# Optimization experiments

Hardware: AMD Instinct MI355X
Metric: run time of the kernel (lower is better)

Reference implementation:

```python
import jax, jax.numpy as jnp
import numpy as np

N_WIN = 7  # winsize in PSF.forward
EMBED_DIM = 3
N_EMBED = 8192

def _box_sum(x, n=N_WIN):
    # sliding-window sum with zero padding == torch ZeroPad2d + unfold sum
    C = x.shape[1]
    k = jnp.ones((C, 1, n, n), x.dtype)
    return jax.lax.conv_general_dilated(
        x, k, (1, 1), [(n // 2, n // 2)] * 2,
        feature_group_count=C, dimension_numbers=('NCHW', 'OIHW', 'NCHW'))

def _patch_stats(x, n=N_WIN):
    # mean / unbiased var over the n*n window (zeros included, matching unfold of zero-padded input)
    N = n * n
    s1 = _box_sum(x, n)
    s2 = _box_sum(x * x, n)
    mean = s1 / N
    var = (s2 - s1 * s1 / N) / (N - 1)  # torch .var default unbiased=True
    return mean, var

def _patch_mv_norm(x, n=N_WIN):
    m, v = _patch_stats(x, n)
    return (x - m) / (jnp.sqrt(v) + 1e-8)

def _conv1x1(x, w, b):
    return jnp.einsum('oi,bihw->bohw', w, x) + b[None, :, None, None]

def _ln(x, g, b, eps=1e-5):
    m = x.mean(-1, keepdims=True)
    v = x.var(-1, keepdims=True)
    return (x - m) / jnp.sqrt(v + eps) * g + b

def _mlp(x, w1, b1, w2, b2):
    h = jax.nn.gelu(x @ w1.T + b1, approximate=True)  # GELU(approximate='tanh')
    return h @ w2.T + b2

def _psf(front, back, e_w, e_b, f_w, f_b, g_w, g_b, h_w, h_b):
    x_norm = _patch_mv_norm(front)
    y_mean, y_var = _patch_stats(back)
    x_adain = x_norm * jnp.sqrt(y_var) + y_mean  # patch_adain (no eps on y_std)
    EE = _conv1x1(x_adain, e_w, e_b)
    FF = _conv1x1(_patch_mv_norm(front), f_w, f_b)
    GG = _conv1x1(_patch_mv_norm(back), g_w, g_b)
    HH = _conv1x1(back, h_w, h_b)
    b, c, h, w = GG.shape
    FFf = FF.reshape(b, c, h * w)
    GGf = GG.reshape(b, c, h * w)
    F_n = jnp.sqrt((FFf * FFf).sum(1))
    G_n = jnp.sqrt((GGf * GGf).sum(1))
    S = (FFf * GGf).sum(1) / (F_n * G_n)          # [b, h*w] cosine similarity
    S_min = S.min(1, keepdims=True)
    S_max = S.max(1, keepdims=True)
    S_n = ((S - S_min) / (S_max - S_min)).reshape(b, 1, h, w)
    return S_n * EE + (1 - S_n) * HH

def reference(front, back, mask, bg_embed,
              mi_w1, mi_b1, mi_w2, mi_b2,
              q_w, k_w, v_w,
              mo_w1, mo_b1, mo_w2, mo_b2,
              n1_g, n1_b, n2_g, n2_b,
              e_w, e_b, f_w, f_b, g_w, g_b, h_w, h_b,
              fuse_w, fuse_b):
    fused = _psf(front, back, e_w, e_b, f_w, f_b, g_w, g_b, h_w, h_b)  # [B,3,H,W]
    B, C, H, W = front.shape
    x = front.reshape(B, C, H * W).transpose(0, 2, 1)   # [B, HW, 3] pixel tokens
    x = _mlp(x, mi_w1, mi_b1, mi_w2, mi_b2)             # mlp_in: 3 -> 6 -> embed_dim
    x = _ln(x, n1_g, n1_b)                              # norm1
    ctx = bg_embed.T                                    # [n_embed, embed_dim] codebook as context
    q = x @ q_w.T                                       # [B, HW, d]
    k = ctx @ k_w.T                                     # [n_embed, d]
    v = ctx @ v_w.T                                     # [n_embed, d]
    scale = q.shape[-1] ** (-0.5)
    attn = jax.nn.softmax(jnp.einsum('bld,nd->bln', q, k) * scale, axis=-1)
    x = jnp.einsum('bln,nd->bld', attn, v)              # [B, HW, d]
    x = _mlp(x, mo_w1, mo_b1, mo_w2, mo_b2)             # mlp_out: d -> 6 -> 3
    x = _ln(x, n2_g, n2_b)                              # norm2
    attn_img = x.transpose(0, 2, 1).reshape(B, 3, H, W)
    out = _conv1x1(jnp.concatenate([attn_img, fused], 1), fuse_w, fuse_b)  # fuse: 6 -> 3
    return out

def setup_inputs() -> dict:
    key = jax.random.key(0)
    ks = jax.random.split(key, 32)
    B, H, W = 2, 96, 96
    d = EMBED_DIM
    n = lambda k, s: jax.random.normal(k, s, dtype=jnp.float32)
    inp = {
        'front': n(ks[0], (B, 3, H, W)),
        'back':  n(ks[1], (B, 3, H, W)),
        'mask':  jax.random.uniform(ks[2], (B, 1, H, W), dtype=jnp.float32),
        'bg_embed': n(ks[3], (d, N_EMBED)),
        'mi_w1': n(ks[4], (6, 3)) * 0.5, 'mi_b1': jnp.zeros((6,)),
        'mi_w2': n(ks[5], (d, 6)) * 0.5, 'mi_b2': jnp.zeros((d,)),
        'q_w': n(ks[6], (d, d)) * 0.5,
        'k_w': n(ks[7], (d, d)) * 0.5,
        'v_w': n(ks[8], (d, d)) * 0.5,
        'mo_w1': n(ks[9], (6, d)) * 0.5, 'mo_b1': jnp.zeros((6,)),
        'mo_w2': n(ks[10], (3, 6)) * 0.5, 'mo_b2': jnp.zeros((3,)),
        'n1_g': jnp.ones((d,)), 'n1_b': jnp.zeros((d,)),
        'n2_g': jnp.ones((3,)), 'n2_b': jnp.zeros((3,)),
        'e_w': n(ks[11], (3, 3)) * 0.3, 'e_b': jnp.zeros((3,)),
        'f_w': n(ks[12], (3, 3)) * 0.3, 'f_b': jnp.zeros((3,)),
        'g_w': n(ks[13], (3, 3)) * 0.3, 'g_b': jnp.zeros((3,)),
        'h_w': n(ks[14], (3, 3)) * 0.3, 'h_b': jnp.zeros((3,)),
        'fuse_w': n(ks[15], (3, 6)) * 0.3, 'fuse_b': jnp.zeros((3,)),
    }
    return inp
```

## Files before the change

### kernel.cpp

```cpp
#include <hip/hip_runtime.h>
#include <math.h>

#define HW    9216
#define NPIX  18432
#define NKEY  8192

#define OFF_Q    0
#define OFF_KV   (OFF_Q + NPIX*4)
#define OFF_EEHS (OFF_KV + NKEY*6)
#define OFF_MM   (OFF_EEHS + NPIX*8)
#define OFF_PART (OFF_MM + 576)

#if __has_builtin(__builtin_amdgcn_exp2f)
#define EXP2(x) __builtin_amdgcn_exp2f(x)
#else
#define EXP2(x) exp2f(x)
#endif

typedef float f32x2 __attribute__((ext_vector_type(2)));
typedef float f32x4 __attribute__((ext_vector_type(4)));

__device__ __forceinline__ f32x2 pk_add(f32x2 a, f32x2 b){
    f32x2 d; asm("v_pk_add_f32 %0, %1, %2" : "=v"(d) : "v"(a), "v"(b)); return d;
}
__device__ __forceinline__ f32x2 pk_mul(f32x2 a, f32x2 b){
    f32x2 d; asm("v_pk_mul_f32 %0, %1, %2" : "=v"(d) : "v"(a), "v"(b)); return d;
}
__device__ __forceinline__ f32x2 pk_fma(f32x2 a, f32x2 b, f32x2 c){
    f32x2 d; asm("v_pk_fma_f32 %0, %1, %2, %3" : "=v"(d) : "v"(a), "v"(b), "v"(c)); return d;
}

__device__ __forceinline__ float gelu_tanh(float x){
    float u = 0.7978845608028654f*(x + 0.044715f*x*x*x);
    return 0.5f*x*(1.0f + tanhf(u));
}

__global__ __launch_bounds__(256) void k1_prep(
    const float* __restrict__ front, const float* __restrict__ back,
    const float* __restrict__ bg,
    const float* __restrict__ k_w,  const float* __restrict__ v_w,
    const float* __restrict__ mi_w1, const float* __restrict__ mi_b1,
    const float* __restrict__ mi_w2, const float* __restrict__ mi_b2,
    const float* __restrict__ q_w,
    const float* __restrict__ n1_g, const float* __restrict__ n1_b,
    const float* __restrict__ e_w,  const float* __restrict__ e_b,
    const float* __restrict__ f_w,  const float* __restrict__ f_b,
    const float* __restrict__ g_w,  const float* __restrict__ g_b,
    const float* __restrict__ h_w,  const float* __restrict__ h_b,
    float* __restrict__ ws)
{
    float* ws_q    = ws + OFF_Q;
    float* ws_kv   = ws + OFF_KV;
    float* ws_eehs = ws + OFF_EEHS;
    float* ws_mm   = ws + OFF_MM;

    __shared__ float lds[6][484];

    int tid = threadIdx.x;
    int bid = blockIdx.x;
    int img = bid / 36;
    int t   = bid % 36;
    int ty  = (t / 6) * 16;
    int tx  = (t % 6) * 16;

    if (bid < 16){
        int p = bid*256 + tid;
        float e00=bg[2*p],        e01=bg[2*p+1];
        float e10=bg[NKEY+2*p],   e11=bg[NKEY+2*p+1];
        float e20=bg[2*NKEY+2*p], e21=bg[2*NKEY+2*p+1];
        float k0[3], k1[3], w0[3], w1[3];
        #pragma unroll
        for (int i=0;i<3;i++){
            k0[i] = k_w[i*3+0]*e00 + k_w[i*3+1]*e10 + k_w[i*3+2]*e20;
            k1[i] = k_w[i*3+0]*e01 + k_w[i*3+1]*e11 + k_w[i*3+2]*e21;
            w0[i] = v_w[i*3+0]*e00 + v_w[i*3+1]*e10 + v_w[i*3+2]*e20;
            w1[i] = v_w[i*3+0]*e01 + v_w[i*3+1]*e11 + v_w[i*3+2]*e21;
        }
        float4* kv4 = (float4*)ws_kv;
        kv4[p*3+0] = make_float4(k0[0],k1[0],k0[1],k1[1]);
        kv4[p*3+1] = make_float4(k0[2],k1[2],w0[0],w1[0]);
        kv4[p*3+2] = make_float4(w0[1],w1[1],w0[2],w1[2]);
    }

    const float* fbase = front + img*3*HW;
    const float* bbase = back  + img*3*HW;

    for (int i = tid; i < 484; i += 256){
        int hy = i / 22, hx = i - hy*22;
        int gy = ty + hy - 3, gx = tx + hx - 3;
        bool ok = ((unsigned)gy < 96u) && ((unsigned)gx < 96u);
        int off = gy*96 + gx;
        #pragma unroll
        for (int c=0;c<3;c++){
            lds[c  ][i] = ok ? fbase[c*HW+off] : 0.0f;
            lds[3+c][i] = ok ? bbase[c*HW+off] : 0.0f;
        }
    }
    __syncthreads();

    int ly = tid / 16, lx = tid - ly*16;
    int y  = ty + ly,  x  = tx + lx;
    int pos = y*96 + x;
    int pix = img*HW + pos;

    float s1f[3]={0,0,0}, s2f[3]={0,0,0}, s1b[3]={0,0,0}, s2b[3]={0,0,0};
    #pragma unroll
    for (int dy=0; dy<7; ++dy){
        int rb = (ly+dy)*22 + lx;
        #pragma unroll
        for (int dx=0; dx<7; ++dx){
            #pragma unroll
            for (int c=0;c<3;c++){
                float fv = lds[c  ][rb+dx];
                float bv = lds[3+c][rb+dx];
                s1f[c]+=fv; s2f[c]+=fv*fv;
                s1b[c]+=bv; s2b[c]+=bv*bv;
            }
        }
    }

    int ctr = (ly+3)*22 + (lx+3);
    float xnf[3], adain[3], bn[3], bval[3], fctr[3];
    #pragma unroll
    for (int c=0;c<3;c++){
        float mf = s1f[c]*(1.0f/49.0f);
        float vf = (s2f[c] - s1f[c]*s1f[c]*(1.0f/49.0f))*(1.0f/48.0f);
        float fv = lds[c][ctr];
        fctr[c] = fv;
        xnf[c] = (fv - mf)/(sqrtf(vf)+1e-8f);

        float mb = s1b[c]*(1.0f/49.0f);
        float vb = (s2b[c] - s1b[c]*s1b[c]*(1.0f/49.0f))*(1.0f/48.0f);
        float bb = lds[3+c][ctr];
        bval[c]  = bb;
        float stdb = sqrtf(vb);
        adain[c] = xnf[c]*stdb + mb;
        bn[c]    = (bb - mb)/(stdb + 1e-8f);
    }

    float EE[3], FF[3], GG[3], HHv[3];
    #pragma unroll
    for (int i=0;i<3;i++){
        EE[i]  = e_w[i*3+0]*adain[0] + e_w[i*3+1]*adain[1] + e_w[i*3+2]*adain[2] + e_b[i];
        FF[i]  = f_w[i*3+0]*xnf[0]   + f_w[i*3+1]*xnf[1]   + f_w[i*3+2]*xnf[2]   + f_b[i];
        GG[i]  = g_w[i*3+0]*bn[0]    + g_w[i*3+1]*bn[1]    + g_w[i*3+2]*bn[2]    + g_b[i];
        HHv[i] = h_w[i*3+0]*bval[0]  + h_w[i*3+1]*bval[1]  + h_w[i*3+2]*bval[2]  + h_b[i];
    }
    float num = FF[0]*GG[0]+FF[1]*GG[1]+FF[2]*GG[2];
    float fn  = sqrtf(FF[0]*FF[0]+FF[1]*FF[1]+FF[2]*FF[2]);
    float gn  = sqrtf(GG[0]*GG[0]+GG[1]*GG[1]+GG[2]*GG[2]);
    float S   = num/(fn*gn);

    float4* eehs4 = (float4*)ws_eehs;
    eehs4[pix*2+0] = make_float4(EE[0],EE[1],EE[2],S);
    eehs4[pix*2+1] = make_float4(HHv[0],HHv[1],HHv[2],0.0f);

    float mn = S, mx = S;
    #pragma unroll
    for (int off=32; off>0; off>>=1){
        mn = fminf(mn, __shfl_xor(mn, off));
        mx = fmaxf(mx, __shfl_xor(mx, off));
    }
    if ((tid & 63) == 0){
        int entry = bid*4 + (tid>>6);
        ws_mm[entry*2+0]=mn; ws_mm[entry*2+1]=mx;
    }

    float xt0 = fctr[0], xt1 = fctr[1], xt2 = fctr[2];
    float h6[6];
    #pragma unroll
    for (int i=0;i<6;i++){
        float a = mi_w1[i*3+0]*xt0 + mi_w1[i*3+1]*xt1 + mi_w1[i*3+2]*xt2 + mi_b1[i];
        h6[i] = gelu_tanh(a);
    }
    float x2[3];
    #pragma unroll
    for (int i=0;i<3;i++){
        float a = mi_b2[i];
        #pragma unroll
        for (int k=0;k<6;k++) a += mi_w2[i*6+k]*h6[k];
        x2[i]=a;
    }
    float m  = (x2[0]+x2[1]+x2[2])*(1.0f/3.0f);
    float d0 = x2[0]-m, d1 = x2[1]-m, d2 = x2[2]-m;
    float var = (d0*d0+d1*d1+d2*d2)*(1.0f/3.0f);
    float inv = 1.0f/sqrtf(var+1e-5f);
    float xn0 = d0*inv*n1_g[0]+n1_b[0];
    float xn1 = d1*inv*n1_g[1]+n1_b[1];
    float xn2 = d2*inv*n1_g[2]+n1_b[2];
    const float qs = 0.5773502691896258f * 1.4426950408889634f;
    float4 qv;
    qv.x = (q_w[0]*xn0 + q_w[1]*xn1 + q_w[2]*xn2)*qs;
    qv.y = (q_w[3]*xn0 + q_w[4]*xn1 + q_w[5]*xn2)*qs;
    qv.z = (q_w[6]*xn0 + q_w[7]*xn1 + q_w[8]*xn2)*qs;
    qv.w = 0.0f;
    ((float4*)ws_q)[pix] = qv;
}


#define DECLQ(J) f32x2 qx##J, qy##J, qz##J; \
                 f32x2 s##J={0.f,0.f}, a0##J={0.f,0.f}, a1##J={0.f,0.f}, a2##J={0.f,0.f};

#define LOADQ(J) { f32x4 qq = q4[qbase + J*256]; \
                   qx##J = (f32x2){qq.x,qq.x}; qy##J = (f32x2){qq.y,qq.y}; qz##J = (f32x2){qq.z,qq.z}; }

#define QSTEP(J) { \
    f32x2 l = pk_fma(qz##J, kz, pk_fma(qy##J, ky, pk_mul(qx##J, kx))); \
    f32x2 p; p.x = EXP2(l.x); p.y = EXP2(l.y); \
    s##J  = pk_add(s##J, p); \
    a0##J = pk_fma(p, v0, a0##J); \
    a1##J = pk_fma(p, v1, a1##J); \
    a2##J = pk_fma(p, v2, a2##J); }

#define STOREP(J) dst[J*256] = (f32x4){s##J.x+s##J.y, a0##J.x+a0##J.y, a1##J.x+a1##J.y, a2##J.x+a2##J.y};

template<int KPC_T>
__global__ __launch_bounds__(256, 4) void k2_attn(const float* __restrict__ ws)
{
    const float* ws_q  = ws + OFF_Q;
    const float* ws_kv = ws + OFF_KV;
    float* ws_part     = (float*)(ws + OFF_PART);

    constexpr int PP = KPC_T/2;
    __shared__ f32x4 lkv[PP*3];
    int tid   = threadIdx.x;
    int chunk = blockIdx.y;
    const f32x4* src = (const f32x4*)ws_kv + (size_t)chunk*PP*3;
    for (int i=tid; i<PP*3; i+=256) lkv[i]=src[i];
    __syncthreads();

    const f32x4* q4 = (const f32x4*)ws_q;
    int qbase = blockIdx.x*(256*4) + tid;

    DECLQ(0) DECLQ(1) DECLQ(2) DECLQ(3)
    LOADQ(0) LOADQ(1) LOADQ(2) LOADQ(3)

    #pragma clang loop distribute(disable)
    for (int kk=0; kk<PP; ++kk){
        f32x4 A = lkv[kk*3+0];
        f32x4 B = lkv[kk*3+1];
        f32x4 C = lkv[kk*3+2];
        f32x2 kx = (f32x2){A.x,A.y}, ky = (f32x2){A.z,A.w}, kz = (f32x2){B.x,B.y};
        f32x2 v0 = (f32x2){B.z,B.w}, v1 = (f32x2){C.x,C.y}, v2 = (f32x2){C.z,C.w};
        QSTEP(0) QSTEP(1) QSTEP(2) QSTEP(3)
    }

    f32x4* dst = (f32x4*)ws_part + (size_t)chunk*NPIX + qbase;
    STOREP(0) STOREP(1) STOREP(2) STOREP(3)
}

template<int NC_T>
__global__ __launch_bounds__(256) void k3_final(
    const float* __restrict__ ws,
    const float* __restrict__ mo_w1, const float* __restrict__ mo_b1,
    const float* __restrict__ mo_w2, const float* __restrict__ mo_b2,
    const float* __restrict__ n2_g,  const float* __restrict__ n2_b,
    const float* __restrict__ fuse_w,const float* __restrict__ fuse_b,
    float* __restrict__ out)
{
    const float* ws_eehs = ws + OFF_EEHS;
    const float* ws_mm   = ws + OFF_MM;
    const float* ws_part = ws + OFF_PART;

    int tid = threadIdx.x;
    int g   = tid >> 6;
    int lp  = tid & 63;
    int pixbase = blockIdx.x*64;
    int pix = pixbase + lp;
    int b   = (pix >= HW) ? 1 : 0;

    constexpr int CPG = NC_T/4;
    float s=0.0f, a0=0.0f, a1=0.0f, a2=0.0f;
    const f32x4* part4 = (const f32x4*)ws_part;
    #pragma unroll 8
    for (int c=g*CPG; c<(g+1)*CPG; ++c){
        f32x4 p = part4[(size_t)c*NPIX + pix];
        s+=p.x; a0+=p.y; a1+=p.z; a2+=p.w;
    }
    __shared__ f32x4 red[256];
    red[tid] = (f32x4){s,a0,a1,a2};

    __shared__ float wmn[4], wmx[4];
    float mn = INFINITY, mx = -INFINITY;
    if (tid < 144){
        mn = ws_mm[(b*144+tid)*2+0];
        mx = ws_mm[(b*144+tid)*2+1];
    }
    #pragma unroll
    for (int off=32; off>0; off>>=1){
        mn = fminf(mn, __shfl_xor(mn, off));
        mx = fmaxf(mx, __shfl_xor(mx, off));
    }
    if ((tid & 63) == 0){ wmn[tid>>6]=mn; wmx[tid>>6]=mx; }
    __syncthreads();

    if (tid < 64){
        mn = fminf(fminf(wmn[0],wmn[1]), fminf(wmn[2],wmn[3]));
        mx = fmaxf(fmaxf(wmx[0],wmx[1]), fmaxf(wmx[2],wmx[3]));

        f32x4 p0 = red[tid], p1 = red[64+tid], p2 = red[128+tid], p3 = red[192+tid];
        s  = p0.x+p1.x+p2.x+p3.x;
        a0 = p0.y+p1.y+p2.y+p3.y;
        a1 = p0.z+p1.z+p2.z+p3.z;
        a2 = p0.w+p1.w+p2.w+p3.w;
        float invs = 1.0f/s;
        float xa0 = a0*invs, xa1 = a1*invs, xa2 = a2*invs;

        float h6[6];
        #pragma unroll
        for (int i=0;i<6;i++){
            float a = mo_w1[i*3+0]*xa0 + mo_w1[i*3+1]*xa1 + mo_w1[i*3+2]*xa2 + mo_b1[i];
            h6[i] = gelu_tanh(a);
        }
        float y[3];
        #pragma unroll
        for (int i=0;i<3;i++){
            float a = mo_b2[i];
            #pragma unroll
            for (int k=0;k<6;k++) a += mo_w2[i*6+k]*h6[k];
            y[i]=a;
        }
        float m  = (y[0]+y[1]+y[2])*(1.0f/3.0f);
        float d0 = y[0]-m, d1 = y[1]-m, d2 = y[2]-m;
        float var = (d0*d0+d1*d1+d2*d2)*(1.0f/3.0f);
        float inv = 1.0f/sqrtf(var+1e-5f);
        float t0 = d0*inv*n2_g[0]+n2_b[0];
        float t1 = d1*inv*n2_g[1]+n2_b[1];
        float t2 = d2*inv*n2_g[2]+n2_b[2];

        float4 e  = ((const float4*)ws_eehs)[pix*2+0];
        float4 hh = ((const float4*)ws_eehs)[pix*2+1];
        float Sn = (e.w - mn)/(mx - mn);
        float f0 = Sn*e.x + (1.0f-Sn)*hh.x;
        float f1 = Sn*e.y + (1.0f-Sn)*hh.y;
        float f2 = Sn*e.z + (1.0f-Sn)*hh.z;

        int pos = pix - b*HW;
        #pragma unroll
        for (int o=0;o<3;o++){
            float val = fuse_b[o]
                      + fuse_w[o*6+0]*t0 + fuse_w[o*6+1]*t1 + fuse_w[o*6+2]*t2
                      + fuse_w[o*6+3]*f0 + fuse_w[o*6+4]*f1 + fuse_w[o*6+5]*f2;
            out[(b*3+o)*HW + pos] = val;
        }
    }
}

extern "C" void kernel_launch(void* const* d_in, const int* in_sizes, int n_in,
                              void* d_out, int out_size, void* d_ws, size_t ws_size,
                              hipStream_t stream) {
    const float* front  = (const float*)d_in[0];
    const float* back   = (const float*)d_in[1];
    const float* bg     = (const float*)d_in[3];
    const float* mi_w1  = (const float*)d_in[4];
    const float* mi_b1  = (const float*)d_in[5];
    const float* mi_w2  = (const float*)d_in[6];
    const float* mi_b2  = (const float*)d_in[7];
    const float* q_w    = (const float*)d_in[8];
    const float* k_w    = (const float*)d_in[9];
    const float* v_w    = (const float*)d_in[10];
    const float* mo_w1  = (const float*)d_in[11];
    const float* mo_b1  = (const float*)d_in[12];
    const float* mo_w2  = (const float*)d_in[13];
    const float* mo_b2  = (const float*)d_in[14];
    const float* n1_g   = (const float*)d_in[15];
    const float* n1_b   = (const float*)d_in[16];
    const float* n2_g   = (const float*)d_in[17];
    const float* n2_b   = (const float*)d_in[18];
    const float* e_w    = (const float*)d_in[19];
    const float* e_b    = (const float*)d_in[20];
    const float* f_w    = (const float*)d_in[21];
    const float* f_b    = (const float*)d_in[22];
    const float* g_w    = (const float*)d_in[23];
    const float* g_b    = (const float*)d_in[24];
    const float* h_w    = (const float*)d_in[25];
    const float* h_b    = (const float*)d_in[26];
    const float* fuse_w = (const float*)d_in[27];
    const float* fuse_b = (const float*)d_in[28];

    float* ws  = (float*)d_ws;
    float* out = (float*)d_out;

    k1_prep<<<dim3(72), 256, 0, stream>>>(
        front, back, bg, k_w, v_w, mi_w1, mi_b1, mi_w2, mi_b2, q_w,
        n1_g, n1_b, e_w, e_b, f_w, f_b, g_w, g_b, h_w, h_b, ws);

    size_t need64 = (size_t)(OFF_PART + 64*NPIX*4) * sizeof(float);
    if (ws_size >= need64){
        k2_attn<128><<<dim3(NPIX/(256*4), 64), 256, 0, stream>>>(ws);
        k3_final<64><<<dim3(NPIX/64), 256, 0, stream>>>(
            ws, mo_w1, mo_b1, mo_w2, mo_b2, n2_g, n2_b, fuse_w, fuse_b, out);
    } else {
        k2_attn<256><<<dim3(NPIX/(256*4), 32), 256, 0, stream>>>(ws);
        k3_final<32><<<dim3(NPIX/64), 256, 0, stream>>>(
            ws, mo_w1, mo_b1, mo_w2, mo_b2, n2_g, n2_b, fuse_w, fuse_b, out);
    }
}
```

Baseline: 57.47 us.

## Compute attention logits with bf16 MFMA using hi/lo split operands

The Q·K dot products in the attention kernel move from packed-FP32 VALU math to `mfma_f32_16x16x32_bf16`. Q and K are stored as bf16 high/low pairs laid out so that a single MFMA computes qh·kh + qh·kl + ql·kh, approximating FP32 accuracy. The exp and value accumulation stay on VALU, followed by cross-lane shuffle reductions. Keys are split into only 4 chunks instead of 64 (or 32), which shrinks the partial-sum traffic that the final kernel reduces. The trade-offs are per-element exps on the MFMA output layout, extra LDS staging with block syncs, and slightly lower precision of the logits.

```diff
diff --git a/kernel.cpp b/kernel.cpp
--- a/kernel.cpp
+++ b/kernel.cpp
@@ -5,9 +5,10 @@
 #define NPIX  18432
 #define NKEY  8192
 
-#define OFF_Q    0
-#define OFF_KV   (OFF_Q + NPIX*4)
-#define OFF_EEHS (OFF_KV + NKEY*6)
+#define OFF_QPK  0
+#define OFF_KPK  (OFF_QPK + NPIX*8)
+#define OFF_VT   (OFF_KPK + NKEY*8)
+#define OFF_EEHS (OFF_VT + NKEY*4)
 #define OFF_MM   (OFF_EEHS + NPIX*8)
 #define OFF_PART (OFF_MM + 576)
 
@@ -17,17 +18,15 @@
 #define EXP2(x) exp2f(x)
 #endif
 
-typedef float f32x2 __attribute__((ext_vector_type(2)));
 typedef float f32x4 __attribute__((ext_vector_type(4)));
-
-__device__ __forceinline__ f32x2 pk_add(f32x2 a, f32x2 b){
-    f32x2 d; asm("v_pk_add_f32 %0, %1, %2" : "=v"(d) : "v"(a), "v"(b)); return d;
-}
-__device__ __forceinline__ f32x2 pk_mul(f32x2 a, f32x2 b){
-    f32x2 d; asm("v_pk_mul_f32 %0, %1, %2" : "=v"(d) : "v"(a), "v"(b)); return d;
-}
-__device__ __forceinline__ f32x2 pk_fma(f32x2 a, f32x2 b, f32x2 c){
-    f32x2 d; asm("v_pk_fma_f32 %0, %1, %2, %3" : "=v"(d) : "v"(a), "v"(b), "v"(c)); return d;
+typedef short bf16x8 __attribute__((ext_vector_type(8)));
+
+__device__ __forceinline__ unsigned bf16rne(float x){
+    unsigned b = __builtin_bit_cast(unsigned, x);
+    return (b + 0x7FFFu + ((b >> 16) & 1u)) >> 16;
+}
+__device__ __forceinline__ float bf16tof(unsigned h){
+    return __builtin_bit_cast(float, h << 16);
 }
 
 __device__ __forceinline__ float gelu_tanh(float x){
@@ -49,8 +48,9 @@
     const float* __restrict__ h_w,  const float* __restrict__ h_b,
     float* __restrict__ ws)
 {
-    float* ws_q    = ws + OFF_Q;
-    float* ws_kv   = ws + OFF_KV;
+    float* ws_qpk  = ws + OFF_QPK;
+    float* ws_kpk  = ws + OFF_KPK;
+    float* ws_vt   = ws + OFF_VT;
     float* ws_eehs = ws + OFF_EEHS;
     float* ws_mm   = ws + OFF_MM;
 
@@ -63,23 +63,31 @@
     int ty  = (t / 6) * 16;
     int tx  = (t % 6) * 16;
 
-    if (bid < 16){
-        int p = bid*256 + tid;
-        float e00=bg[2*p],        e01=bg[2*p+1];
-        float e10=bg[NKEY+2*p],   e11=bg[NKEY+2*p+1];
-        float e20=bg[2*NKEY+2*p], e21=bg[2*NKEY+2*p+1];
-        float k0[3], k1[3], w0[3], w1[3];
+    if (bid < 32){
+        int key = bid*256 + tid;
+        float c0=bg[key], c1=bg[NKEY+key], c2=bg[2*NKEY+key];
+        float kv3[3], vv3[3];
         #pragma unroll
         for (int i=0;i<3;i++){
-            k0[i] = k_w[i*3+0]*e00 + k_w[i*3+1]*e10 + k_w[i*3+2]*e20;
-            k1[i] = k_w[i*3+0]*e01 + k_w[i*3+1]*e11 + k_w[i*3+2]*e21;
-            w0[i] = v_w[i*3+0]*e00 + v_w[i*3+1]*e10 + v_w[i*3+2]*e20;
-            w1[i] = v_w[i*3+0]*e01 + v_w[i*3+1]*e11 + v_w[i*3+2]*e21;
-        }
-        float4* kv4 = (float4*)ws_kv;
-        kv4[p*3+0] = make_float4(k0[0],k1[0],k0[1],k1[1]);
-        kv4[p*3+1] = make_float4(k0[2],k1[2],w0[0],w1[0]);
-        kv4[p*3+2] = make_float4(w0[1],w1[1],w0[2],w1[2]);
+            kv3[i] = k_w[i*3+0]*c0 + k_w[i*3+1]*c1 + k_w[i*3+2]*c2;
+            vv3[i] = v_w[i*3+0]*c0 + v_w[i*3+1]*c1 + v_w[i*3+2]*c2;
+        }
+        unsigned kh[3], kl[3];
+        #pragma unroll
+        for (int i=0;i<3;i++){
+            kh[i] = bf16rne(kv3[i]);
+            kl[i] = bf16rne(kv3[i] - bf16tof(kh[i]));
+        }
+        unsigned u[8];
+        u[0] = kh[0] | (kh[1]<<16);
+        u[1] = kh[2] | (kl[0]<<16);
+        u[2] = kl[1] | (kl[2]<<16);
+        u[3] = kh[0] | (kh[1]<<16);
+        u[4] = kh[2]; u[5]=0; u[6]=0; u[7]=0;
+        f32x4* kp4 = (f32x4*)ws_kpk;
+        kp4[(size_t)key*2+0] = __builtin_bit_cast(f32x4, *(const unsigned __attribute__((ext_vector_type(4)))*)&u[0]);
+        kp4[(size_t)key*2+1] = __builtin_bit_cast(f32x4, *(const unsigned __attribute__((ext_vector_type(4)))*)&u[4]);
+        ((f32x4*)ws_vt)[key] = (f32x4){vv3[0], vv3[1], vv3[2], 0.0f};
     }
 
     const float* fbase = front + img*3*HW;
@@ -189,64 +197,90 @@
     float xn1 = d1*inv*n1_g[1]+n1_b[1];
     float xn2 = d2*inv*n1_g[2]+n1_b[2];
     const float qs = 0.5773502691896258f * 1.4426950408889634f;
-    float4 qv;
-    qv.x = (q_w[0]*xn0 + q_w[1]*xn1 + q_w[2]*xn2)*qs;
-    qv.y = (q_w[3]*xn0 + q_w[4]*xn1 + q_w[5]*xn2)*qs;
-    qv.z = (q_w[6]*xn0 + q_w[7]*xn1 + q_w[8]*xn2)*qs;
-    qv.w = 0.0f;
-    ((float4*)ws_q)[pix] = qv;
-}
-
-
-#define DECLQ(J) f32x2 qx##J, qy##J, qz##J; \
-                 f32x2 s##J={0.f,0.f}, a0##J={0.f,0.f}, a1##J={0.f,0.f}, a2##J={0.f,0.f};
-
-#define LOADQ(J) { f32x4 qq = q4[qbase + J*256]; \
-                   qx##J = (f32x2){qq.x,qq.x}; qy##J = (f32x2){qq.y,qq.y}; qz##J = (f32x2){qq.z,qq.z}; }
-
-#define QSTEP(J) { \
-    f32x2 l = pk_fma(qz##J, kz, pk_fma(qy##J, ky, pk_mul(qx##J, kx))); \
-    f32x2 p; p.x = EXP2(l.x); p.y = EXP2(l.y); \
-    s##J  = pk_add(s##J, p); \
-    a0##J = pk_fma(p, v0, a0##J); \
-    a1##J = pk_fma(p, v1, a1##J); \
-    a2##J = pk_fma(p, v2, a2##J); }
-
-#define STOREP(J) dst[J*256] = (f32x4){s##J.x+s##J.y, a0##J.x+a0##J.y, a1##J.x+a1##J.y, a2##J.x+a2##J.y};
-
-template<int KPC_T>
-__global__ __launch_bounds__(256, 4) void k2_attn(const float* __restrict__ ws)
+    float qv[3];
+    qv[0] = (q_w[0]*xn0 + q_w[1]*xn1 + q_w[2]*xn2)*qs;
+    qv[1] = (q_w[3]*xn0 + q_w[4]*xn1 + q_w[5]*xn2)*qs;
+    qv[2] = (q_w[6]*xn0 + q_w[7]*xn1 + q_w[8]*xn2)*qs;
+
+    unsigned qh[3], ql[3];
+    #pragma unroll
+    for (int i=0;i<3;i++){
+        qh[i] = bf16rne(qv[i]);
+        ql[i] = bf16rne(qv[i] - bf16tof(qh[i]));
+    }
+    unsigned u[8];
+    u[0] = qh[0] | (qh[1]<<16);
+    u[1] = qh[2] | (qh[0]<<16);
+    u[2] = qh[1] | (qh[2]<<16);
+    u[3] = ql[0] | (ql[1]<<16);
+    u[4] = ql[2]; u[5]=0; u[6]=0; u[7]=0;
+    f32x4* qp4 = (f32x4*)ws_qpk;
+    qp4[(size_t)pix*2+0] = __builtin_bit_cast(f32x4, *(const unsigned __attribute__((ext_vector_type(4)))*)&u[0]);
+    qp4[(size_t)pix*2+1] = __builtin_bit_cast(f32x4, *(const unsigned __attribute__((ext_vector_type(4)))*)&u[4]);
+}
+
+#define RED4(vv, mm) { vv.x += __shfl_xor(vv.x,mm); vv.y += __shfl_xor(vv.y,mm); \
+                       vv.z += __shfl_xor(vv.z,mm); vv.w += __shfl_xor(vv.w,mm); }
+
+__global__ __launch_bounds__(256) void k2_attn(const float* __restrict__ ws)
 {
-    const float* ws_q  = ws + OFF_Q;
-    const float* ws_kv = ws + OFF_KV;
-    float* ws_part     = (float*)(ws + OFF_PART);
-
-    constexpr int PP = KPC_T/2;
-    __shared__ f32x4 lkv[PP*3];
-    int tid   = threadIdx.x;
-    int chunk = blockIdx.y;
-    const f32x4* src = (const f32x4*)ws_kv + (size_t)chunk*PP*3;
-    for (int i=tid; i<PP*3; i+=256) lkv[i]=src[i];
-    __syncthreads();
-
-    const f32x4* q4 = (const f32x4*)ws_q;
-    int qbase = blockIdx.x*(256*4) + tid;
-
-    DECLQ(0) DECLQ(1) DECLQ(2) DECLQ(3)
-    LOADQ(0) LOADQ(1) LOADQ(2) LOADQ(3)
-
-    #pragma clang loop distribute(disable)
-    for (int kk=0; kk<PP; ++kk){
-        f32x4 A = lkv[kk*3+0];
-        f32x4 B = lkv[kk*3+1];
-        f32x4 C = lkv[kk*3+2];
-        f32x2 kx = (f32x2){A.x,A.y}, ky = (f32x2){A.z,A.w}, kz = (f32x2){B.x,B.y};
-        f32x2 v0 = (f32x2){B.z,B.w}, v1 = (f32x2){C.x,C.y}, v2 = (f32x2){C.z,C.w};
-        QSTEP(0) QSTEP(1) QSTEP(2) QSTEP(3)
-    }
-
-    f32x4* dst = (f32x4*)ws_part + (size_t)chunk*NPIX + qbase;
-    STOREP(0) STOREP(1) STOREP(2) STOREP(3)
+    const f32x4* qpk = (const f32x4*)(ws + OFF_QPK);
+    const f32x4* kpk = (const f32x4*)(ws + OFF_KPK);
+    const f32x4* vt  = (const f32x4*)(ws + OFF_VT);
+    f32x4* part      = (f32x4*)(ws + OFF_PART);
+
+    __shared__ f32x4 lkp[1024];
+    __shared__ f32x4 lv[512];
+
+    int tid  = threadIdx.x;
+    int bid  = blockIdx.x;
+    int kq   = bid & 3;
+    int qg   = bid >> 2;
+    int wave = tid >> 6, lane = tid & 63;
+    int qtile = qg*4 + wave;
+    int g = lane >> 4, col = lane & 15;
+
+    bf16x8 afrag = {0,0,0,0,0,0,0,0};
+    if (g < 2)
+        afrag = __builtin_bit_cast(bf16x8, qpk[(size_t)(qtile*16 + col)*2 + g]);
+
+    f32x4 s_ = {0,0,0,0}, a0_ = {0,0,0,0}, a1_ = {0,0,0,0}, a2_ = {0,0,0,0};
+
+    const f32x4* kpbase = kpk + (size_t)(kq*2048)*2;
+    const f32x4* vbase  = vt + kq*2048;
+
+    for (int chunk=0; chunk<4; ++chunk){
+        for (int i=tid; i<1024; i+=256) lkp[i] = kpbase[chunk*1024 + i];
+        for (int i=tid; i<512;  i+=256) lv[i]  = vbase[chunk*512 + i];
+        __syncthreads();
+        #pragma unroll 4
+        for (int st=0; st<32; ++st){
+            bf16x8 bfrag = {0,0,0,0,0,0,0,0};
+            if (g < 2)
+                bfrag = __builtin_bit_cast(bf16x8, lkp[(st*16+col)*2 + g]);
+            f32x4 S = __builtin_amdgcn_mfma_f32_16x16x32_bf16(afrag, bfrag, (f32x4){0,0,0,0}, 0, 0, 0);
+            f32x4 v = lv[st*16+col];
+            f32x4 p;
+            p.x = EXP2(S.x); p.y = EXP2(S.y); p.z = EXP2(S.z); p.w = EXP2(S.w);
+            s_  += p;
+            a0_ += p * v.x;
+            a1_ += p * v.y;
+            a2_ += p * v.z;
+        }
+        __syncthreads();
+    }
+
+    RED4(s_, 8) RED4(a0_, 8) RED4(a1_, 8) RED4(a2_, 8)
+    RED4(s_, 4) RED4(a0_, 4) RED4(a1_, 4) RED4(a2_, 4)
+    RED4(s_, 2) RED4(a0_, 2) RED4(a1_, 2) RED4(a2_, 2)
+    RED4(s_, 1) RED4(a0_, 1) RED4(a1_, 1) RED4(a2_, 1)
+
+    int qbase = qtile*16 + g*4;
+    f32x4* dst = part + (size_t)kq*NPIX + qbase;
+    if      (col==0) dst[0] = (f32x4){s_.x, a0_.x, a1_.x, a2_.x};
+    else if (col==1) dst[1] = (f32x4){s_.y, a0_.y, a1_.y, a2_.y};
+    else if (col==2) dst[2] = (f32x4){s_.z, a0_.z, a1_.z, a2_.z};
+    else if (col==3) dst[3] = (f32x4){s_.w, a0_.w, a1_.w, a2_.w};
 }
 
 template<int NC_T>
@@ -272,7 +306,7 @@
     constexpr int CPG = NC_T/4;
     float s=0.0f, a0=0.0f, a1=0.0f, a2=0.0f;
     const f32x4* part4 = (const f32x4*)ws_part;
-    #pragma unroll 8
+    #pragma unroll
     for (int c=g*CPG; c<(g+1)*CPG; ++c){
         f32x4 p = part4[(size_t)c*NPIX + pix];
         s+=p.x; a0+=p.y; a1+=p.z; a2+=p.w;
@@ -385,14 +419,8 @@
         front, back, bg, k_w, v_w, mi_w1, mi_b1, mi_w2, mi_b2, q_w,
         n1_g, n1_b, e_w, e_b, f_w, f_b, g_w, g_b, h_w, h_b, ws);
 
-    size_t need64 = (size_t)(OFF_PART + 64*NPIX*4) * sizeof(float);
-    if (ws_size >= need64){
-        k2_attn<128><<<dim3(NPIX/(256*4), 64), 256, 0, stream>>>(ws);
-        k3_final<64><<<dim3(NPIX/64), 256, 0, stream>>>(
-            ws, mo_w1, mo_b1, mo_w2, mo_b2, n2_g, n2_b, fuse_w, fuse_b, out);
-    } else {
-        k2_attn<256><<<dim3(NPIX/(256*4), 32), 256, 0, stream>>>(ws);
-        k3_final<32><<<dim3(NPIX/64), 256, 0, stream>>>(
-            ws, mo_w1, mo_b1, mo_w2, mo_b2, n2_g, n2_b, fuse_w, fuse_b, out);
-    }
-}
+    k2_attn<<<dim3(1152), 256, 0, stream>>>(ws);
+
+    k3_final<4><<<dim3(NPIX/64), 256, 0, stream>>>(
+        ws, mo_w1, mo_b1, mo_w2, mo_b2, n2_g, n2_b, fuse_w, fuse_b, out);
+}
```

Measured after the change: 56.92 us. About the same (-0.9%).
